# Performance work log

Hardware: AMD Instinct MI355X
Metric: run time of the kernel (lower is better)

## Reference

```python
import math
import jax, jax.numpy as jnp
import numpy as np

IMG_SIZE = 2048
STRIDE = 8
NUM_CLASSES = 80
TOPK = 1000
CONF_THRESH = 0.05
NMS_THRESH = 0.6
CTR_CLAMP = 32.0
SCALE_CLAMP = math.log(1000.0 / 16)
ANCHOR_SIZES = np.array([[32,32],[64,32],[32,64],[64,64],[128,64],[64,128],[128,128],[256,128],[128,256]], dtype=np.float32)


def make_anchors():
    fmp = IMG_SIZE // STRIDE  # 256
    yy, xx = np.meshgrid(np.arange(fmp), np.arange(fmp), indexing='ij')
    xy = (np.stack([xx, yy], axis=-1).reshape(-1, 2).astype(np.float32) + 0.5) * STRIDE  # [fmp*fmp, 2]
    na = ANCHOR_SIZES.shape[0]
    xy = np.repeat(xy[:, None, :], na, axis=1)           # [fmp*fmp, na, 2]
    wh = np.tile(ANCHOR_SIZES[None, :, :], (fmp * fmp, 1, 1))  # [fmp*fmp, na, 2]
    return jnp.asarray(np.concatenate([xy, wh], axis=-1).reshape(-1, 4))  # [M, 4]


def setup_inputs() -> dict:
    key = jax.random.key(0)
    k1, k2 = jax.random.split(key)
    M = (IMG_SIZE // STRIDE) ** 2 * ANCHOR_SIZES.shape[0]
    cls_pred = jax.random.normal(k1, (M, NUM_CLASSES), dtype=jnp.float32) * 2.0 - 2.0
    reg_pred = jax.random.normal(k2, (M, 4), dtype=jnp.float32) * 0.5
    anchor_boxes = make_anchors()
    return {"cls_pred": cls_pred, "reg_pred": reg_pred, "anchor_boxes": anchor_boxes}


def decode_boxes(anchors, reg):
    # anchors, reg: [N, 4] (cx, cy, w, h) / (dx, dy, dw, dh)
    ctr_off = jnp.clip(reg[..., :2] * anchors[..., 2:], -CTR_CLAMP, CTR_CLAMP)
    ctr = anchors[..., :2] + ctr_off
    wh = anchors[..., 2:] * jnp.exp(jnp.minimum(reg[..., 2:], SCALE_CLAMP))
    return jnp.concatenate([ctr - 0.5 * wh, ctr + 0.5 * wh], axis=-1)


def iou_matrix(boxes):
    # boxes: [N, 4] x1y1x2y2 -> [N, N] IoU, matching the numpy NMS math
    x1, y1, x2, y2 = boxes[:, 0], boxes[:, 1], boxes[:, 2], boxes[:, 3]
    areas = (x2 - x1) * (y2 - y1)
    xx1 = jnp.maximum(x1[:, None], x1[None, :])
    yy1 = jnp.maximum(y1[:, None], y1[None, :])
    xx2 = jnp.minimum(x2[:, None], x2[None, :])
    yy2 = jnp.minimum(y2[:, None], y2[None, :])
    w = jnp.maximum(1e-10, xx2 - xx1)
    h = jnp.maximum(1e-10, yy2 - yy1)
    inter = w * h
    return inter / (areas[:, None] + areas[None, :] - inter + 1e-10)


def reference(cls_pred, reg_pred, anchor_boxes):
    # per-anchor best class score/label
    probs = jax.nn.sigmoid(cls_pred)                 # [M, C]
    scores_all = jnp.max(probs, axis=-1)             # [M]
    labels_all = jnp.argmax(probs, axis=-1)          # [M]
    # top-k filtering (scores sorted descending)
    scores, idx = jax.lax.top_k(scores_all, TOPK)    # [K]
    labels = labels_all[idx]
    reg = reg_pred[idx]
    anch = anchor_boxes[idx]
    # decode + normalize
    bboxes = jnp.clip(decode_boxes(anch, reg) / IMG_SIZE, 0.0, 1.0)  # [K, 4]
    valid = scores >= CONF_THRESH                    # conf filter as mask (fixed shape)
    # per-class greedy NMS: candidates are score-sorted, so greedy order = index order
    iou = iou_matrix(bboxes)                         # [K, K]
    same_cls = labels[:, None] == labels[None, :]    # [K, K]
    suppress_mat = (iou > NMS_THRESH) & same_cls     # j suppresses i if kept, same class, earlier
    idx_range = jnp.arange(TOPK)

    def body(i, keep):
        earlier_kept_overlap = jnp.any(keep & suppress_mat[:, i] & (idx_range < i))
        return keep.at[i].set(valid[i] & ~earlier_kept_overlap)

    keep = jax.lax.fori_loop(0, TOPK, body, jnp.zeros(TOPK, dtype=bool))
    return bboxes, scores, labels, keep
```

## Files before the change

### kernel.cpp

```cpp
#include <hip/hip_runtime.h>
#include <math.h>

#define M_ANCH   589824
#define NCLS     80
#define TOPK_N   1000
#define CAND_CAP 4096
#define NREP     16
#define NBIN     8192
#define KSHIFT   19

#define SCALE_CLAMP_F 4.135166556742356f
#define INV_IMG       (1.0f/2048.0f)

#define WS_H1R     0
#define WS_CNT     524288
#define WS_GBIN    524292
#define WS_MEMSET  524296
#define WS_CAND    524544
#define WS_BOXES   557312
#define WS_LABELS  573312
#define WS_VALID   577312
#define WS_SUP     581376
#define WS_MKEYS   709632

__device__ __forceinline__ unsigned fmap(unsigned b) {
    return (b & 0x80000000u) ? ~b : (b | 0x80000000u);
}
__device__ __forceinline__ unsigned funmap(unsigned k) {
    return (k & 0x80000000u) ? (k ^ 0x80000000u) : ~k;
}

__global__ __launch_bounds__(256) void k_rowmax(const float* __restrict__ cls,
                                                unsigned* __restrict__ mkeys,
                                                unsigned* __restrict__ h1r) {
    __shared__ unsigned lh[NBIN];
    int t = threadIdx.x;
    for (int b = t; b < NBIN; b += 256) lh[b] = 0;
    __syncthreads();
    int lane = t & 63, w = t >> 6;
    int part = lane & 3;
    int rsub = (w << 4) + (lane >> 2);
#pragma unroll
    for (int it = 0; it < 16; ++it) {
        int row = blockIdx.x * 1024 + it * 64 + rsub;
        const float4* p = (const float4*)(cls + (size_t)row * NCLS) + part * 5;
        float m = -INFINITY;
#pragma unroll
        for (int i = 0; i < 5; ++i) {
            float4 v = p[i];
            m = fmaxf(m, fmaxf(fmaxf(v.x, v.y), fmaxf(v.z, v.w)));
        }
        m = fmaxf(m, __shfl_xor(m, 1));
        m = fmaxf(m, __shfl_xor(m, 2));
        if (part == 0) {
            unsigned key = fmap(__float_as_uint(m));
            mkeys[row] = key;
            atomicAdd(&lh[key >> KSHIFT], 1u);
        }
    }
    __syncthreads();
    unsigned rep = (blockIdx.x & (NREP - 1)) * NBIN;
    for (int b = t; b < NBIN; b += 256) {
        unsigned c = lh[b];
        if (c) atomicAdd(&h1r[rep + b], c);
    }
}

__global__ __launch_bounds__(256) void k_find(const unsigned* __restrict__ h1r,
                                              unsigned* __restrict__ gbin) {
    __shared__ unsigned hist[NBIN];
    __shared__ unsigned csum[256];
    int t = threadIdx.x;
    for (int b = t; b < NBIN; b += 256) {
        unsigned s = 0;
        for (int r = 0; r < NREP; ++r) s += h1r[r * NBIN + b];
        hist[b] = s;
    }
    __syncthreads();
    unsigned cs = 0;
    for (int k = 0; k < 32; ++k) cs += hist[t * 32 + k];
    csum[t] = cs;
    __syncthreads();
    if (t == 0) {
        unsigned cum = 0, above = 0;
        int C = 0;
        for (int c = 255; c >= 0; --c) {
            if (cum + csum[c] >= TOPK_N || c == 0) { C = c; above = cum; break; }
            cum += csum[c];
        }
        int B = C * 32;
        unsigned cum2 = above;
        for (int b = C * 32 + 31; b >= C * 32; --b) {
            cum2 += hist[b];
            if (cum2 >= TOPK_N) { B = b; break; }
            if (b == C * 32) B = b;
        }
        *gbin = (B >= 1) ? (unsigned)(B - 1) : 0u;
    }
}

__global__ __launch_bounds__(256) void k_gather(const unsigned* __restrict__ mkeys,
                                                const unsigned* __restrict__ gbin,
                                                unsigned* __restrict__ cnt,
                                                unsigned long long* __restrict__ cand) {
    int i = blockIdx.x * blockDim.x + threadIdx.x;
    if (i >= M_ANCH) return;
    unsigned gb = *gbin;
    unsigned key = mkeys[i];
    if ((key >> KSHIFT) >= gb) {
        unsigned pos = atomicAdd(cnt, 1u);
        if (pos < CAND_CAP) {
            float m = __uint_as_float(funmap(key));
            float e = (float)exp(-(double)m);
            float sc = 1.0f / (1.0f + e);
            unsigned sb = __float_as_uint(sc);
            cand[pos] = ((unsigned long long)sb << 32) | (unsigned)(~(unsigned)i);
        }
    }
}

__global__ __launch_bounds__(256) void k_rank_decode(const unsigned* __restrict__ cnt,
                                                     const unsigned long long* __restrict__ cand,
                                                     const float* __restrict__ cls,
                                                     const float* __restrict__ reg,
                                                     const float* __restrict__ anch,
                                                     float* __restrict__ out,
                                                     float4* __restrict__ boxes_ws,
                                                     int* __restrict__ lab_ws,
                                                     int* __restrict__ val_ws) {
    __shared__ unsigned long long sh[CAND_CAP];
    int t = threadIdx.x;
    unsigned n = *cnt;
    if (n > CAND_CAP) n = CAND_CAP;
    for (int k = t; k < (int)n; k += 256) sh[k] = cand[k];
    __syncthreads();
    int k = blockIdx.x * 256 + t;
    if (k >= (int)n) return;
    unsigned long long key = sh[k];
    int rank = 0;
    for (int j = 0; j < (int)n; ++j) rank += (sh[j] > key) ? 1 : 0;
    if (rank >= TOPK_N) return;
    int r = rank;
    unsigned idx = ~(unsigned)(key & 0xFFFFFFFFull);
    float sc = __uint_as_float((unsigned)(key >> 32));
    const float* row = cls + (size_t)idx * NCLS;
    float best = -INFINITY;
    int lbl = 0;
    for (int c = 0; c < NCLS; ++c) {
        float v = row[c];
        if (v > best) { best = v; lbl = c; }
    }
    float4 rg = ((const float4*)reg)[idx];
    float4 an = ((const float4*)anch)[idx];
    float ox = fminf(fmaxf(rg.x * an.z, -32.0f), 32.0f);
    float oy = fminf(fmaxf(rg.y * an.w, -32.0f), 32.0f);
    float cx = an.x + ox, cy = an.y + oy;
    float w = an.z * expf(fminf(rg.z, SCALE_CLAMP_F));
    float h = an.w * expf(fminf(rg.w, SCALE_CLAMP_F));
    float x1 = fminf(fmaxf((cx - 0.5f * w) * INV_IMG, 0.0f), 1.0f);
    float y1 = fminf(fmaxf((cy - 0.5f * h) * INV_IMG, 0.0f), 1.0f);
    float x2 = fminf(fmaxf((cx + 0.5f * w) * INV_IMG, 0.0f), 1.0f);
    float y2 = fminf(fmaxf((cy + 0.5f * h) * INV_IMG, 0.0f), 1.0f);
    out[r * 4 + 0] = x1;
    out[r * 4 + 1] = y1;
    out[r * 4 + 2] = x2;
    out[r * 4 + 3] = y2;
    out[4 * TOPK_N + r] = sc;
    out[5 * TOPK_N + r] = (float)lbl;
    boxes_ws[r] = make_float4(x1, y1, x2, y2);
    lab_ws[r] = lbl;
    val_ws[r] = (sc >= 0.05f) ? 1 : 0;
}

__global__ __launch_bounds__(64) void k_sup(const float4* __restrict__ boxes,
                                            const int* __restrict__ labs,
                                            unsigned long long* __restrict__ sup) {
    int i = blockIdx.x;
    int lane = threadIdx.x;
    float4 bi = boxes[i];
    float ai = (bi.z - bi.x) * (bi.w - bi.y);
    int li = labs[i];
#pragma unroll
    for (int c = 0; c < 16; ++c) {
        int j = c * 64 + lane;
        bool bit = false;
        if (j < TOPK_N) {
            float4 bj = boxes[j];
            float aj = (bj.z - bj.x) * (bj.w - bj.y);
            float xx1 = fmaxf(bi.x, bj.x), yy1 = fmaxf(bi.y, bj.y);
            float xx2 = fminf(bi.z, bj.z), yy2 = fminf(bi.w, bj.w);
            float w = fmaxf(1e-10f, xx2 - xx1);
            float h = fmaxf(1e-10f, yy2 - yy1);
            float inter = w * h;
            float iou = inter / (ai + aj - inter + 1e-10f);
            bit = (iou > 0.6f) && (labs[j] == li);
        }
        unsigned long long ball = __ballot(bit);
        if (lane == 0) sup[(size_t)i * 16 + c] = ball;
    }
}

__global__ __launch_bounds__(64) void k_nms(const unsigned long long* __restrict__ sup,
                                            const int* __restrict__ val,
                                            float* __restrict__ out_keep) {
    int lane = threadIdx.x;
    unsigned long long kw[16];
#pragma unroll
    for (int c = 0; c < 16; ++c) kw[c] = 0ull;
    unsigned long long lowmask = (lane == 0) ? 0ull : (~0ull >> (64 - lane));
    for (int c = 0; c < 16; ++c) {
        int b = c * 64 + lane;
        bool v = false;
        bool ext = false;
        unsigned long long m = 0ull;
        if (b < TOPK_N) {
            v = (val[b] != 0);
            const unsigned long long* rowp = sup + (size_t)b * 16;
            for (int w = 0; w < c; ++w) ext = ext || ((rowp[w] & kw[w]) != 0ull);
            m = rowp[c];
        }
        bool mykeep = false;
        for (int i = 0; i < 64; ++i) {
            unsigned long long ball = __ballot(mykeep);
            if (lane == i) {
                mykeep = v && !ext && ((ball & m & lowmask) == 0ull);
            }
        }
        unsigned long long ball = __ballot(mykeep);
        kw[c] = ball;
        if (b < TOPK_N) out_keep[b] = ((ball >> lane) & 1ull) ? 1.0f : 0.0f;
    }
}

extern "C" void kernel_launch(void* const* d_in, const int* in_sizes, int n_in,
                              void* d_out, int out_size, void* d_ws, size_t ws_size,
                              hipStream_t stream) {
    const float* cls  = (const float*)d_in[0];
    const float* reg  = (const float*)d_in[1];
    const float* anch = (const float*)d_in[2];
    float* out = (float*)d_out;
    char* ws = (char*)d_ws;

    unsigned* h1r  = (unsigned*)(ws + WS_H1R);
    unsigned* cnt  = (unsigned*)(ws + WS_CNT);
    unsigned* gbin = (unsigned*)(ws + WS_GBIN);
    unsigned long long* cand = (unsigned long long*)(ws + WS_CAND);
    float4* boxes = (float4*)(ws + WS_BOXES);
    int* labs     = (int*)(ws + WS_LABELS);
    int* valid    = (int*)(ws + WS_VALID);
    unsigned long long* sup = (unsigned long long*)(ws + WS_SUP);
    unsigned* mkeys = (unsigned*)(ws + WS_MKEYS);

    hipMemsetAsync(ws, 0, WS_MEMSET, stream);

    k_rowmax<<<M_ANCH / 1024, 256, 0, stream>>>(cls, mkeys, h1r);
    k_find  <<<1, 256, 0, stream>>>(h1r, gbin);
    k_gather<<<M_ANCH / 256, 256, 0, stream>>>(mkeys, gbin, cnt, cand);
    k_rank_decode<<<CAND_CAP / 256, 256, 0, stream>>>(cnt, cand, cls, reg, anch,
                                                      out, boxes, labs, valid);
    k_sup   <<<TOPK_N, 64, 0, stream>>>(boxes, labs, sup);
    k_nms   <<<1, 64, 0, stream>>>(sup, valid, out + 6 * TOPK_N);
}
```

Baseline: 439.1 us.

## Retune rowmax grid, widen find, vectorize gather, trim sup and NMS work

k_rowmax now processes 256 rows per block, giving four times as many blocks for more parallelism. In exchange each block pays a full 8192-bin shared histogram clear and flush. k_find uses 1024 threads to reduce the replicated histograms. k_gather reads eight keys per thread and does one aggregated atomic, cutting atomic contention. k_sup computes only the lower-triangular chunks that NMS reads, and k_nms skips the serial 64-step ballot loop when a chunk has no in-chunk suppression.

```diff
diff --git a/kernel.cpp b/kernel.cpp
--- a/kernel.cpp
+++ b/kernel.cpp
@@ -41,8 +41,8 @@
     int part = lane & 3;
     int rsub = (w << 4) + (lane >> 2);
 #pragma unroll
-    for (int it = 0; it < 16; ++it) {
-        int row = blockIdx.x * 1024 + it * 64 + rsub;
+    for (int it = 0; it < 4; ++it) {
+        int row = blockIdx.x * 256 + it * 64 + rsub;
         const float4* p = (const float4*)(cls + (size_t)row * NCLS) + part * 5;
         float m = -INFINITY;
 #pragma unroll
@@ -66,20 +66,23 @@
     }
 }
 
-__global__ __launch_bounds__(256) void k_find(const unsigned* __restrict__ h1r,
-                                              unsigned* __restrict__ gbin) {
+__global__ __launch_bounds__(1024) void k_find(const unsigned* __restrict__ h1r,
+                                               unsigned* __restrict__ gbin) {
     __shared__ unsigned hist[NBIN];
     __shared__ unsigned csum[256];
     int t = threadIdx.x;
-    for (int b = t; b < NBIN; b += 256) {
+    for (int b = t; b < NBIN; b += 1024) {
         unsigned s = 0;
+#pragma unroll
         for (int r = 0; r < NREP; ++r) s += h1r[r * NBIN + b];
         hist[b] = s;
     }
     __syncthreads();
-    unsigned cs = 0;
-    for (int k = 0; k < 32; ++k) cs += hist[t * 32 + k];
-    csum[t] = cs;
+    if (t < 256) {
+        unsigned cs = 0;
+        for (int k = 0; k < 32; ++k) cs += hist[t * 32 + k];
+        csum[t] = cs;
+    }
     __syncthreads();
     if (t == 0) {
         unsigned cum = 0, above = 0;
@@ -99,22 +102,32 @@
     }
 }
 
-__global__ __launch_bounds__(256) void k_gather(const unsigned* __restrict__ mkeys,
+__global__ __launch_bounds__(256) void k_gather(const uint4* __restrict__ mk4,
                                                 const unsigned* __restrict__ gbin,
                                                 unsigned* __restrict__ cnt,
                                                 unsigned long long* __restrict__ cand) {
-    int i = blockIdx.x * blockDim.x + threadIdx.x;
-    if (i >= M_ANCH) return;
+    int tid = blockIdx.x * 256 + threadIdx.x;
     unsigned gb = *gbin;
-    unsigned key = mkeys[i];
-    if ((key >> KSHIFT) >= gb) {
-        unsigned pos = atomicAdd(cnt, 1u);
-        if (pos < CAND_CAP) {
-            float m = __uint_as_float(funmap(key));
-            float e = (float)exp(-(double)m);
-            float sc = 1.0f / (1.0f + e);
-            unsigned sb = __float_as_uint(sc);
-            cand[pos] = ((unsigned long long)sb << 32) | (unsigned)(~(unsigned)i);
+    uint4 a = mk4[tid * 2];
+    uint4 b4 = mk4[tid * 2 + 1];
+    unsigned keys[8] = {a.x, a.y, a.z, a.w, b4.x, b4.y, b4.z, b4.w};
+    int lc = 0;
+    unsigned sel[8];
+#pragma unroll
+    for (int q = 0; q < 8; ++q)
+        if ((keys[q] >> KSHIFT) >= gb) sel[lc++] = (unsigned)q;
+    if (lc) {
+        unsigned base = atomicAdd(cnt, (unsigned)lc);
+        for (int q = 0; q < lc; ++q) {
+            unsigned pos = base + (unsigned)q;
+            if (pos < CAND_CAP) {
+                unsigned i = (unsigned)tid * 8u + sel[q];
+                float m = __uint_as_float(funmap(keys[sel[q]]));
+                float e = (float)exp(-(double)m);
+                float sc = 1.0f / (1.0f + e);
+                cand[pos] = ((unsigned long long)__float_as_uint(sc) << 32)
+                            | (unsigned)(~i);
+            }
         }
     }
 }
@@ -177,11 +190,11 @@
                                             unsigned long long* __restrict__ sup) {
     int i = blockIdx.x;
     int lane = threadIdx.x;
+    int cmax = i >> 6;
     float4 bi = boxes[i];
     float ai = (bi.z - bi.x) * (bi.w - bi.y);
     int li = labs[i];
-#pragma unroll
-    for (int c = 0; c < 16; ++c) {
+    for (int c = 0; c <= cmax; ++c) {
         int j = c * 64 + lane;
         bool bit = false;
         if (j < TOPK_N) {
@@ -219,16 +232,20 @@
             for (int w = 0; w < c; ++w) ext = ext || ((rowp[w] & kw[w]) != 0ull);
             m = rowp[c];
         }
-        bool mykeep = false;
-        for (int i = 0; i < 64; ++i) {
-            unsigned long long ball = __ballot(mykeep);
-            if (lane == i) {
-                mykeep = v && !ext && ((ball & m & lowmask) == 0ull);
+        unsigned long long inchunk = m & lowmask;
+        bool mykeep;
+        if (__ballot(inchunk != 0ull) == 0ull) {
+            mykeep = v && !ext;
+        } else {
+            mykeep = false;
+            for (int i = 0; i < 64; ++i) {
+                unsigned long long ball = __ballot(mykeep);
+                if (lane == i) mykeep = v && !ext && ((ball & inchunk) == 0ull);
             }
         }
-        unsigned long long ball = __ballot(mykeep);
-        kw[c] = ball;
-        if (b < TOPK_N) out_keep[b] = ((ball >> lane) & 1ull) ? 1.0f : 0.0f;
+        unsigned long long ball2 = __ballot(mykeep);
+        kw[c] = ball2;
+        if (b < TOPK_N) out_keep[b] = ((ball2 >> lane) & 1ull) ? 1.0f : 0.0f;
     }
 }
 
@@ -253,9 +270,9 @@
 
     hipMemsetAsync(ws, 0, WS_MEMSET, stream);
 
-    k_rowmax<<<M_ANCH / 1024, 256, 0, stream>>>(cls, mkeys, h1r);
-    k_find  <<<1, 256, 0, stream>>>(h1r, gbin);
-    k_gather<<<M_ANCH / 256, 256, 0, stream>>>(mkeys, gbin, cnt, cand);
+    k_rowmax<<<M_ANCH / 256, 256, 0, stream>>>(cls, mkeys, h1r);
+    k_find  <<<1, 1024, 0, stream>>>(h1r, gbin);
+    k_gather<<<M_ANCH / (256 * 8), 256, 0, stream>>>((const uint4*)mkeys, gbin, cnt, cand);
     k_rank_decode<<<CAND_CAP / 256, 256, 0, stream>>>(cnt, cand, cls, reg, anch,
                                                       out, boxes, labs, valid);
     k_sup   <<<TOPK_N, 64, 0, stream>>>(boxes, labs, sup);
```

Result: faster. 386.0 us (-12.1%).
